# Kernel optimization log

Measured on AMD Instinct MI355X. Metric: run time of the kernel, lower is better.

## Reference

```python
import jax, jax.numpy as jnp
import numpy as np

HID = 256
VOC = 50257
N_E_SH = 2
N_E_SP = 2
N_MB = 4
B, S = 8, 512
LN_EPS = 1e-3  # keras LayerNormalization default epsilon
STD = 0.02


def setup_inputs() -> dict:
    key = jax.random.key(0)
    ks = jax.random.split(key, 10)
    x = jax.random.normal(ks[0], (B, S, HID), dtype=jnp.float32)
    # labels drawn in [1, VOC) so the `labels > 0` mask keeps every token (static shape)
    labels = jax.random.randint(ks[1], (B, S), 1, VOC, dtype=jnp.int32)
    xb = jax.random.randint(ks[2], (B, S), 0, N_MB + 1, dtype=jnp.int32)
    W_sh = jax.random.normal(ks[3], (N_E_SH, HID, HID), dtype=jnp.float32) * STD
    b_sh = jax.random.normal(ks[4], (N_E_SH, HID), dtype=jnp.float32) * STD
    W_sp = jax.random.normal(ks[5], (N_MB * N_E_SP, HID, HID), dtype=jnp.float32) * STD
    b_sp = jax.random.normal(ks[6], (N_MB * N_E_SP, HID), dtype=jnp.float32) * STD
    w_gates = jax.random.normal(ks[7], (N_MB, HID, N_E_SH + N_E_SP), dtype=jnp.float32) * STD
    vocab_bias = jax.random.normal(ks[8], (VOC,), dtype=jnp.float32) * STD
    emb = jax.random.normal(ks[9], (VOC, HID), dtype=jnp.float32) * STD  # tied_to.weights[0]
    ln_gamma = jnp.ones((HID,), dtype=jnp.float32)
    ln_beta = jnp.zeros((HID,), dtype=jnp.float32)
    return {"x": x, "labels": labels, "xb": xb, "W_sh": W_sh, "b_sh": b_sh,
            "W_sp": W_sp, "b_sp": b_sp, "w_gates": w_gates,
            "vocab_bias": vocab_bias, "emb": emb,
            "ln_gamma": ln_gamma, "ln_beta": ln_beta}


def _layernorm(h, gamma, beta):
    mu = jnp.mean(h, axis=-1, keepdims=True)
    var = jnp.mean(jnp.square(h - mu), axis=-1, keepdims=True)
    return gamma * (h - mu) * jax.lax.rsqrt(var + LN_EPS) + beta


def reference(x, labels, xb, W_sh, b_sh, W_sp, b_sp, w_gates, vocab_bias, emb, ln_gamma, ln_beta):
    xf = x.reshape(-1, HID)          # [N, H]
    lf = labels.reshape(-1)          # [N], all > 0 => mask gather is identity
    xbf = xb.reshape(-1)             # [N]

    # shared + branch-specific experts: [e, N, H]
    sh = jnp.einsum('nd,edh->enh', xf, W_sh) + b_sh[:, None, :]
    sp = jnp.einsum('nd,edh->enh', xf, W_sp) + b_sp[:, None, :]
    sp = sp.reshape(N_MB, N_E_SP, -1, HID)                       # [t, e_sp, N, H]
    sh_b = jnp.broadcast_to(sh[None], (N_MB, N_E_SH, sh.shape[1], HID))
    merge = jnp.concatenate([sh_b, sp], axis=1)                  # [t, e, N, H]

    gates = jax.nn.softmax(jnp.einsum('nd,tde->tne', xf, w_gates), axis=-1)  # [t, N, e]
    out = jnp.einsum('tend,tne->tnd', merge, gates)              # [t, N, H]

    outputs = jnp.concatenate([jnp.zeros_like(xf)[None], out], axis=0)  # [t+1, N, H]
    oh = jax.nn.one_hot(xbf, N_MB + 1, dtype=jnp.float32)        # [N, t+1]
    e_out = jnp.einsum('tnd,nt->nd', outputs, oh)                # [N, H]

    e_out = _layernorm(e_out, ln_gamma, ln_beta) + xf

    logits = e_out @ emb.T + vocab_bias                          # [N, VOC]
    logp = jax.nn.log_softmax(logits, axis=-1)
    loss = -jnp.take_along_axis(logp, lf[:, None], axis=-1)[:, 0]  # [N]
    prob = jnp.exp(logp)
    return prob, loss
```

## Files before the change

kernel.cpp:

```cpp
#include <hip/hip_runtime.h>

#define HID 256
#define VOC 50257
#define NTOK 4096
#define NCT3 393
#define CG 8
#define TN 128
#define LN_EPS 1e-3f
#define PROB_ELEMS 205852672

typedef __attribute__((ext_vector_type(8))) short bf16x8;
typedef __attribute__((ext_vector_type(4))) float f32x4;
typedef __attribute__((ext_vector_type(16))) float f32x16;

__device__ inline unsigned short f2bf(float f) {
    unsigned int u = __builtin_bit_cast(unsigned int, f);
    unsigned int r = u + 0x7FFFu + ((u >> 16) & 1u);
    return (unsigned short)(r >> 16);
}
__device__ inline float bf2f(unsigned short b) {
    unsigned int u = ((unsigned int)b) << 16;
    return __builtin_bit_cast(float, u);
}

__global__ __launch_bounds__(256) void prep_kernel(
    const float* __restrict__ emb, const float* __restrict__ Wsh,
    const float* __restrict__ Wsp,
    unsigned short* __restrict__ embbf, unsigned short* __restrict__ Wtbf) {
    __shared__ float t[64][65];
    int tid = threadIdx.x;
    if (blockIdx.x < 160) {
        int bx = blockIdx.x % 40, by = blockIdx.x / 40;
        int gcol0 = bx * 64;
        int k0 = by * 64;
        int e = gcol0 >> 8, h0 = gcol0 & 255;
        const float* Wp = (e < 2) ? (Wsh + e * 65536) : (Wsp + (e - 2) * 65536);
#pragma unroll
        for (int i = 0; i < 16; ++i) {
            int id = tid + i * 256;
            int k = id >> 6, h = id & 63;
            t[k][h] = Wp[(k0 + k) * 256 + h0 + h];
        }
        __syncthreads();
#pragma unroll
        for (int i = 0; i < 4; ++i) {
            int id = tid + i * 256;
            int h = id >> 4, kq = id & 15;
            ushort4 o;
            o.x = f2bf(t[kq * 4 + 0][h]); o.y = f2bf(t[kq * 4 + 1][h]);
            o.z = f2bf(t[kq * 4 + 2][h]); o.w = f2bf(t[kq * 4 + 3][h]);
            *reinterpret_cast<ushort4*>(Wtbf + (size_t)(gcol0 + h) * 256 + k0 + kq * 4) = o;
        }
    } else {
        const int n4 = VOC * HID / 4;
        int i = (blockIdx.x - 160) * 256 + tid;
        int stride = (gridDim.x - 160) * 256;
        for (; i < n4; i += stride) {
            float4 v = reinterpret_cast<const float4*>(emb)[i];
            ushort4 o;
            o.x = f2bf(v.x); o.y = f2bf(v.y); o.z = f2bf(v.z); o.w = f2bf(v.w);
            reinterpret_cast<ushort4*>(embbf)[i] = o;
        }
    }
}

__global__ __launch_bounds__(256) void expert_gemm(
    const float* __restrict__ x,
    const unsigned short* __restrict__ Wtbf,
    const float* __restrict__ bsh, const float* __restrict__ bsp,
    float* __restrict__ cexp) {
    __shared__ unsigned short sA[64 * 256];
    __shared__ unsigned short sB[64 * 256];
    int bid = blockIdx.x;
    int rt = bid & 63;
    int ct = bid >> 6;
    int row0 = rt * 64, col0 = ct * 64;
    int tid = threadIdx.x;

#pragma unroll
    for (int i = 0; i < 8; ++i) {
        int id = tid + i * 256;
        int r = id >> 5, c = id & 31;
        const float* xr = x + (size_t)(row0 + r) * 256 + c * 8;
        float4 v0 = *reinterpret_cast<const float4*>(xr);
        float4 v1 = *reinterpret_cast<const float4*>(xr + 4);
        bf16x8 o;
        o[0] = (short)f2bf(v0.x); o[1] = (short)f2bf(v0.y);
        o[2] = (short)f2bf(v0.z); o[3] = (short)f2bf(v0.w);
        o[4] = (short)f2bf(v1.x); o[5] = (short)f2bf(v1.y);
        o[6] = (short)f2bf(v1.z); o[7] = (short)f2bf(v1.w);
        *reinterpret_cast<bf16x8*>(sA + r * 256 + ((c ^ (r & 7)) * 8)) = o;
    }
#pragma unroll
    for (int i = 0; i < 8; ++i) {
        int id = tid + i * 256;
        int j = id >> 5, c = id & 31;
        bf16x8 v = *reinterpret_cast<const bf16x8*>(Wtbf + (size_t)(col0 + j) * 256 + c * 8);
        *reinterpret_cast<bf16x8*>(sB + j * 256 + ((c ^ (j & 7)) * 8)) = v;
    }
    __syncthreads();

    int lane = tid & 63, wave = tid >> 6;
    int wcol = wave * 16;
    int lrow = lane & 15, g = lane >> 4;
    f32x4 zero4 = {0.f, 0.f, 0.f, 0.f};
    f32x4 acc[4];
#pragma unroll
    for (int mf = 0; mf < 4; ++mf) acc[mf] = zero4;

#pragma unroll
    for (int ks = 0; ks < 8; ++ks) {
        int kc = ks * 4 + g;
        int j = wcol + lrow;
        bf16x8 b = *reinterpret_cast<const bf16x8*>(sB + j * 256 + ((kc ^ (j & 7)) * 8));
        bf16x8 a[4];
#pragma unroll
        for (int mf = 0; mf < 4; ++mf) {
            int r = mf * 16 + lrow;
            a[mf] = *reinterpret_cast<const bf16x8*>(sA + r * 256 + ((kc ^ (r & 7)) * 8));
        }
#pragma unroll
        for (int mf = 0; mf < 4; ++mf)
            acc[mf] = __builtin_amdgcn_mfma_f32_16x16x32_bf16(a[mf], b, acc[mf], 0, 0, 0);
    }

    {
        int col = col0 + wcol + lrow;
        int e = col >> 8, h = col & 255;
        float bias = (e < 2) ? bsh[e * 256 + h] : bsp[(e - 2) * 256 + h];
#pragma unroll
        for (int mf = 0; mf < 4; ++mf)
#pragma unroll
            for (int r = 0; r < 4; ++r) {
                int row = row0 + mf * 16 + g * 4 + r;
                cexp[(size_t)row * 2560 + col] = acc[mf][r] + bias;
            }
    }
}

__global__ __launch_bounds__(256) void combine_ln(
    const float* __restrict__ x, const int* __restrict__ xb,
    const float* __restrict__ wg, const float* __restrict__ cexp,
    const float* __restrict__ gamma, const float* __restrict__ beta,
    unsigned short* __restrict__ ebf) {
    __shared__ float sx[256];
    __shared__ float sg[4];
    __shared__ float rs[4], rq[4];
    int n = blockIdx.x, h = threadIdx.x;
    float xv = x[n * 256 + h];
    sx[h] = xv;
    __syncthreads();
    int xbn = xb[n];
    float eo;
    if (xbn == 0) {
        eo = beta[h] + xv;
    } else {
        int t = xbn - 1;
        int wv = h >> 6, lane = h & 63;
        float p = 0.f;
        const float* wgt = wg + t * 1024;
#pragma unroll
        for (int i = 0; i < 4; ++i) {
            int d = lane * 4 + i;
            p += sx[d] * wgt[d * 4 + wv];
        }
#pragma unroll
        for (int off = 32; off; off >>= 1) p += __shfl_down(p, off);
        if (lane == 0) sg[wv] = p;
        __syncthreads();
        float g0 = sg[0], g1 = sg[1], g2 = sg[2], g3 = sg[3];
        float mx = fmaxf(fmaxf(g0, g1), fmaxf(g2, g3));
        float e0 = __expf(g0 - mx), e1 = __expf(g1 - mx);
        float e2 = __expf(g2 - mx), e3 = __expf(g3 - mx);
        float inv = 1.f / (e0 + e1 + e2 + e3);
        const float* cr = cexp + (size_t)n * 2560;
        float o = (e0 * cr[h] + e1 * cr[256 + h] +
                   e2 * cr[512 + t * 512 + h] + e3 * cr[768 + t * 512 + h]) * inv;
        float s = o, q = o * o;
#pragma unroll
        for (int off = 32; off; off >>= 1) { s += __shfl_down(s, off); q += __shfl_down(q, off); }
        if (lane == 0) { rs[wv] = s; rq[wv] = q; }
        __syncthreads();
        float mu = (rs[0] + rs[1] + rs[2] + rs[3]) * (1.f / 256.f);
        float ex2 = (rq[0] + rq[1] + rq[2] + rq[3]) * (1.f / 256.f);
        float var = ex2 - mu * mu;
        eo = gamma[h] * (o - mu) * rsqrtf(var + LN_EPS) + beta[h] + xv;
    }
    ebf[n * 256 + h] = f2bf(eo);
}

template <int PASS>
__global__ __launch_bounds__(512, 2) void big_gemm(
    const unsigned short* __restrict__ ebf,
    const unsigned short* __restrict__ embbf,
    const float* __restrict__ vbias,
    float* __restrict__ psum,
    const float* __restrict__ denom,
    float* __restrict__ prob) {
    __shared__ unsigned short sB[2][TN * 256];

    int bid = blockIdx.x;
    int rt = bid >> 3;
    int cg = bid & 7;
    int row0 = rt * 128;
    int tid = threadIdx.x;
    int wave = tid >> 6, lane = tid & 63;
    int l31 = lane & 31, hi = lane >> 5;
    int wr = wave >> 2, wc = wave & 3;
    int tstart = (cg * NCT3) / CG;
    int tend = ((cg + 1) * NCT3) / CG;
    int nmy = tend - tstart;

    bf16x8 a[2][16];
    {
        const unsigned short* ab =
            ebf + (size_t)(row0 + wr * 64 + l31) * 256 + hi * 8;
#pragma unroll
        for (int mf = 0; mf < 2; ++mf)
#pragma unroll
            for (int ks = 0; ks < 16; ++ks)
                a[mf][ks] = *reinterpret_cast<const bf16x8*>(ab + mf * 32 * 256 + ks * 16);
    }

    auto stage = [&](int ct, int buf) {
        int col0 = ct * TN;
#pragma unroll
        for (int i = 0; i < 8; ++i) {
            int col = i * 16 + wave * 2 + hi;
            int gcol = col0 + col; if (gcol >= VOC) gcol = VOC - 1;
            const unsigned short* src =
                embbf + (size_t)gcol * 256 + ((l31 ^ (col & 7)) * 8);
            unsigned short* dst = (unsigned short*)sB[buf] + (size_t)(i * 512 + wave * 64) * 8;
            __builtin_amdgcn_global_load_lds(
                (const __attribute__((address_space(1))) void*)src,
                (__attribute__((address_space(3))) void*)dst, 16, 0, 0);
        }
    };

    stage(tstart, 0);
    asm volatile("s_waitcnt vmcnt(0)" ::: "memory");
    __syncthreads();

    float invd[2][16];
    if (PASS == 1) {
#pragma unroll
        for (int mf = 0; mf < 2; ++mf)
#pragma unroll
            for (int r = 0; r < 16; ++r) {
                int row = row0 + wr * 64 + mf * 32 + (r & 3) + 8 * (r >> 2) + 4 * hi;
                invd[mf][r] = 1.f / denom[row];
            }
    }
    float es[2][16];
    if (PASS == 0) {
#pragma unroll
        for (int mf = 0; mf < 2; ++mf)
#pragma unroll
            for (int r = 0; r < 16; ++r) es[mf][r] = 0.f;
    }

    f32x16 zz = {0.f,0.f,0.f,0.f,0.f,0.f,0.f,0.f,0.f,0.f,0.f,0.f,0.f,0.f,0.f,0.f};

    for (int it = 0; it < nmy; ++it) {
        int ct = tstart + it;
        if (it + 1 < nmy) stage(ct + 1, (it + 1) & 1);

        int gc = ct * TN + wc * 32 + l31;
        float bvb;
        if (PASS == 0) bvb = (gc < VOC) ? vbias[gc] : -1e4f;
        else           bvb = vbias[(gc < VOC) ? gc : (VOC - 1)];

        const unsigned short* sBc = (const unsigned short*)sB[it & 1];
        int bcol = wc * 32 + l31;
        f32x16 c0 = zz, c1 = zz;
#pragma unroll
        for (int ks = 0; ks < 16; ++ks) {
            int kc = ks * 2 + hi;
            bf16x8 b = *reinterpret_cast<const bf16x8*>(
                sBc + bcol * 256 + ((kc ^ (bcol & 7)) * 8));
            c0 = __builtin_amdgcn_mfma_f32_32x32x16_bf16(a[0][ks], b, c0, 0, 0, 0);
            c1 = __builtin_amdgcn_mfma_f32_32x32x16_bf16(a[1][ks], b, c1, 0, 0, 0);
        }

        if (PASS == 0) {
#pragma unroll
            for (int r = 0; r < 16; ++r) {
                es[0][r] += __expf(c0[r] + bvb);
                es[1][r] += __expf(c1[r] + bvb);
            }
        } else {
#pragma unroll
            for (int r = 0; r < 16; ++r) {
                c0[r] = __expf(c0[r] + bvb) * invd[0][r];
                c1[r] = __expf(c1[r] + bvb) * invd[1][r];
            }
        }

        asm volatile("s_waitcnt vmcnt(0)" ::: "memory");
        __syncthreads();

        if (PASS == 1) {
            if (gc < VOC) {
#pragma unroll
                for (int r = 0; r < 16; ++r) {
                    int rowr = row0 + wr * 64 + (r & 3) + 8 * (r >> 2) + 4 * hi;
                    prob[(size_t)rowr * VOC + gc] = c0[r];
                    prob[(size_t)(rowr + 32) * VOC + gc] = c1[r];
                }
            }
        }
    }

    if (PASS == 0) {
#pragma unroll
        for (int mf = 0; mf < 2; ++mf)
#pragma unroll
            for (int r = 0; r < 16; ++r) {
                float v = es[mf][r];
#pragma unroll
                for (int off = 1; off < 32; off <<= 1) v += __shfl_xor(v, off);
                if (l31 == 0) {
                    int row = row0 + wr * 64 + mf * 32 + (r & 3) + 8 * (r >> 2) + 4 * hi;
                    psum[(size_t)row * 32 + cg * 4 + wc] = v;
                }
            }
    }
}

__global__ __launch_bounds__(64) void finalize_k(
    const float* __restrict__ psum,
    const unsigned short* __restrict__ ebf, const unsigned short* __restrict__ embbf,
    const float* __restrict__ vbias, const int* __restrict__ labels,
    float* __restrict__ denom, float* __restrict__ loss) {
    int n = blockIdx.x, lane = threadIdx.x;
    float s = (lane < 32) ? psum[(size_t)n * 32 + lane] : 0.f;
#pragma unroll
    for (int off = 1; off < 32; off <<= 1) s += __shfl_xor(s, off);
    int lf = labels[n];
    const unsigned short* ev = ebf + n * 256;
    const unsigned short* mv = embbf + (size_t)lf * 256;
    float p = 0.f;
#pragma unroll
    for (int i = 0; i < 4; ++i) p += bf2f(ev[lane * 4 + i]) * bf2f(mv[lane * 4 + i]);
#pragma unroll
    for (int off = 1; off < 64; off <<= 1) p += __shfl_xor(p, off);
    if (lane == 0) {
        denom[n] = s;
        loss[n] = logf(s) - (p + vbias[lf]);
    }
}

extern "C" void kernel_launch(void* const* d_in, const int* in_sizes, int n_in,
                              void* d_out, int out_size, void* d_ws, size_t ws_size,
                              hipStream_t stream) {
    const float* x      = (const float*)d_in[0];
    const int*   labels = (const int*)d_in[1];
    const int*   xb     = (const int*)d_in[2];
    const float* Wsh    = (const float*)d_in[3];
    const float* bsh    = (const float*)d_in[4];
    const float* Wsp    = (const float*)d_in[5];
    const float* bsp    = (const float*)d_in[6];
    const float* wg     = (const float*)d_in[7];
    const float* vbias  = (const float*)d_in[8];
    const float* emb    = (const float*)d_in[9];
    const float* gamma  = (const float*)d_in[10];
    const float* beta   = (const float*)d_in[11];

    char* ws = (char*)d_ws;
    unsigned short* embbf = (unsigned short*)(ws + 2097152);
    unsigned short* Wtbf  = (unsigned short*)(ws + 27828736);
    float* cexp           = (float*)(ws + 29360128);
    unsigned short* ebf   = (unsigned short*)(ws + 71303168);
    float* psum           = (float*)(ws + 73400320);
    float* denom          = (float*)(ws + 73924608);

    float* prob = (float*)d_out;
    float* loss = prob + PROB_ELEMS;

    prep_kernel<<<dim3(2208), dim3(256), 0, stream>>>(emb, Wsh, Wsp, embbf, Wtbf);
    expert_gemm<<<dim3(64 * 40), dim3(256), 0, stream>>>(x, Wtbf, bsh, bsp, cexp);
    combine_ln<<<dim3(NTOK), dim3(256), 0, stream>>>(x, xb, wg, cexp, gamma, beta, ebf);
    big_gemm<0><<<dim3(256), dim3(512), 0, stream>>>(ebf, embbf, vbias, psum, nullptr, nullptr);
    finalize_k<<<dim3(NTOK), dim3(64), 0, stream>>>(psum, ebf, embbf, vbias, labels, denom, loss);
    big_gemm<1><<<dim3(256), dim3(512), 0, stream>>>(ebf, embbf, vbias, nullptr, denom, prob);
}
```

Baseline: 535.1 us.

## Replace second logits GEMM pass with bf16 exp buffer and scaling kernel

The vocab GEMM now runs once. It accumulates the softmax denominators and also writes the unnormalized exponentials as bf16 into a large workspace buffer. A new row-wise kernel then reads that buffer, divides by the denominator and writes the fp32 probabilities, so the second full GEMM pass is no longer needed. The cost is an extra round trip of several hundred MB through HBM, and the probabilities lose accuracy because they are rounded to bf16 before normalization. The new path runs only when the workspace is large enough; otherwise the old two-pass path is kept.

```diff
diff --git a/kernel.cpp b/kernel.cpp
--- a/kernel.cpp
+++ b/kernel.cpp
@@ -6,11 +6,13 @@
 #define NCT3 393
 #define CG 8
 #define TN 128
+#define EPITCH 50304
 #define LN_EPS 1e-3f
 #define PROB_ELEMS 205852672
 
 typedef __attribute__((ext_vector_type(8))) short bf16x8;
 typedef __attribute__((ext_vector_type(4))) float f32x4;
+typedef __attribute__((ext_vector_type(4), aligned(4))) float f32x4u;
 typedef __attribute__((ext_vector_type(16))) float f32x16;
 
 __device__ inline unsigned short f2bf(float f) {
@@ -196,7 +198,8 @@
     const float* __restrict__ vbias,
     float* __restrict__ psum,
     const float* __restrict__ denom,
-    float* __restrict__ prob) {
+    float* __restrict__ prob,
+    unsigned short* __restrict__ ebuf) {
     __shared__ unsigned short sB[2][TN * 256];
 
     int bid = blockIdx.x;
@@ -252,7 +255,7 @@
             }
     }
     float es[2][16];
-    if (PASS == 0) {
+    if (PASS != 1) {
 #pragma unroll
         for (int mf = 0; mf < 2; ++mf)
 #pragma unroll
@@ -267,7 +270,7 @@
 
         int gc = ct * TN + wc * 32 + l31;
         float bvb;
-        if (PASS == 0) bvb = (gc < VOC) ? vbias[gc] : -1e4f;
+        if (PASS != 1) bvb = (gc < VOC) ? vbias[gc] : -1e4f;
         else           bvb = vbias[(gc < VOC) ? gc : (VOC - 1)];
 
         const unsigned short* sBc = (const unsigned short*)sB[it & 1];
@@ -288,6 +291,14 @@
                 es[0][r] += __expf(c0[r] + bvb);
                 es[1][r] += __expf(c1[r] + bvb);
             }
+        } else if (PASS == 2) {
+#pragma unroll
+            for (int r = 0; r < 16; ++r) {
+                c0[r] = __expf(c0[r] + bvb);
+                c1[r] = __expf(c1[r] + bvb);
+                es[0][r] += c0[r];
+                es[1][r] += c1[r];
+            }
         } else {
 #pragma unroll
             for (int r = 0; r < 16; ++r) {
@@ -308,10 +319,20 @@
                     prob[(size_t)(rowr + 32) * VOC + gc] = c1[r];
                 }
             }
-        }
-    }
-
-    if (PASS == 0) {
+        } else if (PASS == 2) {
+            if (gc < VOC) {
+                unsigned short* eb = ebuf + gc;
+#pragma unroll
+                for (int r = 0; r < 16; ++r) {
+                    int rowr = row0 + wr * 64 + (r & 3) + 8 * (r >> 2) + 4 * hi;
+                    eb[(size_t)rowr * EPITCH] = f2bf(c0[r]);
+                    eb[(size_t)(rowr + 32) * EPITCH] = f2bf(c1[r]);
+                }
+            }
+        }
+    }
+
+    if (PASS != 1) {
 #pragma unroll
         for (int mf = 0; mf < 2; ++mf)
 #pragma unroll
@@ -348,6 +369,31 @@
         denom[n] = s;
         loss[n] = logf(s) - (p + vbias[lf]);
     }
+}
+
+__global__ __launch_bounds__(256) void scale_prob(
+    const unsigned short* __restrict__ ebuf, const float* __restrict__ denom,
+    float* __restrict__ prob) {
+    int row = blockIdx.x;
+    float inv = 1.f / denom[row];
+    const unsigned short* src = ebuf + (size_t)row * EPITCH;
+    float* dst = prob + (size_t)row * VOC;
+    int t = threadIdx.x;
+#pragma unroll 4
+    for (int it = 0; it < 24; ++it) {
+        int off = it * 2048 + t * 8;
+        bf16x8 v = *reinterpret_cast<const bf16x8*>(src + off);
+        f32x4 o0, o1;
+#pragma unroll
+        for (int j = 0; j < 4; ++j) {
+            o0[j] = bf2f((unsigned short)v[j]) * inv;
+            o1[j] = bf2f((unsigned short)v[4 + j]) * inv;
+        }
+        *reinterpret_cast<f32x4u*>(dst + off) = o0;
+        *reinterpret_cast<f32x4u*>(dst + off + 4) = o1;
+    }
+    for (int off = 49152 + t; off < VOC; off += 256)
+        dst[off] = bf2f(src[off]) * inv;
 }
 
 extern "C" void kernel_launch(void* const* d_in, const int* in_sizes, int n_in,
@@ -373,6 +419,9 @@
     unsigned short* ebf   = (unsigned short*)(ws + 71303168);
     float* psum           = (float*)(ws + 73400320);
     float* denom          = (float*)(ws + 73924608);
+    unsigned short* ebuf  = (unsigned short*)(ws + 73990144);
+
+    const size_t WS_NEED = 73990144ull + 412090368ull;
 
     float* prob = (float*)d_out;
     float* loss = prob + PROB_ELEMS;
@@ -380,7 +429,14 @@
     prep_kernel<<<dim3(2208), dim3(256), 0, stream>>>(emb, Wsh, Wsp, embbf, Wtbf);
     expert_gemm<<<dim3(64 * 40), dim3(256), 0, stream>>>(x, Wtbf, bsh, bsp, cexp);
     combine_ln<<<dim3(NTOK), dim3(256), 0, stream>>>(x, xb, wg, cexp, gamma, beta, ebf);
-    big_gemm<0><<<dim3(256), dim3(512), 0, stream>>>(ebf, embbf, vbias, psum, nullptr, nullptr);
-    finalize_k<<<dim3(NTOK), dim3(64), 0, stream>>>(psum, ebf, embbf, vbias, labels, denom, loss);
-    big_gemm<1><<<dim3(256), dim3(512), 0, stream>>>(ebf, embbf, vbias, nullptr, denom, prob);
-}
+
+    if (ws_size >= WS_NEED) {
+        big_gemm<2><<<dim3(256), dim3(512), 0, stream>>>(ebf, embbf, vbias, psum, nullptr, nullptr, ebuf);
+        finalize_k<<<dim3(NTOK), dim3(64), 0, stream>>>(psum, ebf, embbf, vbias, labels, denom, loss);
+        scale_prob<<<dim3(NTOK), dim3(256), 0, stream>>>(ebuf, denom, prob);
+    } else {
+        big_gemm<0><<<dim3(256), dim3(512), 0, stream>>>(ebf, embbf, vbias, psum, nullptr, nullptr, nullptr);
+        finalize_k<<<dim3(NTOK), dim3(64), 0, stream>>>(psum, ebf, embbf, vbias, labels, denom, loss);
+        big_gemm<1><<<dim3(256), dim3(512), 0, stream>>>(ebf, embbf, vbias, nullptr, denom, prob, nullptr);
+    }
+}
```

After: 544.1 us. Within noise of the previous version (+1.7%).
